# Kernel optimization log

Hardware: AMD Instinct MI355X
Metric: run time of the kernel (lower is better)

The kernel has to match this reference:

```python
import jax, jax.numpy as jnp
import numpy as np

B, T, E, H = 4, 1024, 512, 8


def setup_inputs() -> dict:
    key = jax.random.key(0)
    ks = jax.random.split(key, 8)
    s = 1.0 / np.sqrt(E)
    return {
        "x": jax.random.normal(ks[0], (B, T, E), dtype=jnp.float32),
        "mask": jnp.zeros((B, T, T), dtype=jnp.float32),
        "Wk": jax.random.uniform(ks[1], (H * E, E), minval=-s, maxval=s, dtype=jnp.float32),
        "Wq": jax.random.uniform(ks[2], (H * E, E), minval=-s, maxval=s, dtype=jnp.float32),
        "Wv": jax.random.uniform(ks[3], (H * E, E), minval=-s, maxval=s, dtype=jnp.float32),
        "Wu": jax.random.uniform(ks[4], (E, H * E), minval=-s, maxval=s, dtype=jnp.float32),
        "bu": jnp.zeros((E,), dtype=jnp.float32),
        "heads": H,
    }


def reference(x, mask, Wk, Wq, Wv, Wu, bu, heads):
    b, t, e = x.shape
    h = heads
    # Projections: torch Linear computes x @ W.T; output features laid out as [h, e]
    k = (x @ Wk.T).reshape(b, t, h, e).transpose(0, 2, 1, 3)  # [b,h,t,e]
    q = (x @ Wq.T).reshape(b, t, h, e).transpose(0, 2, 1, 3)
    v = (x @ Wv.T).reshape(b, t, h, e).transpose(0, 2, 1, 3)
    dot = jnp.einsum("bhqe,bhke->bhqk", q, k) / jnp.sqrt(jnp.float32(e))
    # mask repeat_interleave over b*h == broadcast over heads; subtracted additively
    att = jax.nn.softmax(dot - mask[:, None, :, :], axis=-1)
    out = jnp.einsum("bhqk,bhke->bhqe", att, v)  # [b,h,t,e]
    out = out.transpose(0, 2, 1, 3).reshape(b, t, h * e)
    return out @ Wu.T + bu
```

## Files before the change

kernel.cpp:

```cpp
#include <hip/hip_runtime.h>
#include <hip/hip_bf16.h>


typedef short bf16x8 __attribute__((ext_vector_type(8)));
typedef float f32x4 __attribute__((ext_vector_type(4)));
typedef unsigned short u16x8 __attribute__((ext_vector_type(8)));

__device__ __forceinline__ unsigned short f2bf(float f) {
  unsigned int u = __float_as_uint(f);
  u += 0x7FFFu + ((u >> 16) & 1u);
  return (unsigned short)(u >> 16);
}
__device__ __forceinline__ float bf2f(unsigned short s) {
  return __uint_as_float(((unsigned int)s) << 16);
}

typedef const __attribute__((address_space(1))) unsigned int* gas1_t;
typedef __attribute__((address_space(3))) unsigned int* las3_t;

__device__ __forceinline__ void gload16(const unsigned short* g, unsigned short* l) {
  __builtin_amdgcn_global_load_lds((gas1_t)g, (las3_t)l, 16, 0, 0);
}

__device__ __forceinline__ void store_val(unsigned short* p, float v) { *p = f2bf(v); }
__device__ __forceinline__ void store_val(float* p, float v) { *p = v; }

template<typename OutT>
__global__ __launch_bounds__(512, 1) void gemm_bt2(
    const unsigned short* __restrict__ A, const unsigned short* __restrict__ B,
    OutT* __restrict__ C,
    int K, int lda, int ldb, int ldc, int zshift,
    long long sAb, long long sAh, long long sBb, long long sBh,
    long long sCb, long long sCh, float alpha)
{
  const int tid  = threadIdx.x;
  const int lane = tid & 63;
  const int wave = tid >> 6;
  const int l15 = lane & 15, lhi = lane >> 4;
  const int wm = wave >> 2, wn = wave & 3;

  const int nx = gridDim.x, nxy = gridDim.x * gridDim.y;
  const int nwg = nxy * gridDim.z;
  int flat = blockIdx.x + nx * blockIdx.y + nxy * blockIdx.z;
  flat = (flat & 7) * (nwg >> 3) + (flat >> 3);
  const int bz = flat / nxy;
  const int rem = flat - bz * nxy;
  const int by = rem / nx;
  const int bx = rem - by * nx;

  const int bb = bz >> zshift, hh = bz & ((1 << zshift) - 1);
  const long long m0 = (long long)by * 256;
  const long long n0 = (long long)bx * 256;

  const unsigned short* Ab = A + bb * sAb + hh * sAh;
  const unsigned short* Bb = B + bb * sBb + hh * sBh;

  __shared__ __align__(16) unsigned short lds[49152];

  const unsigned short* gA[2];
  const unsigned short* gB[2];
  int fidx[2];
#pragma unroll
  for (int c = 0; c < 2; ++c) {
    const int f = c * 8 + wave;
    fidx[c] = f;
    gA[c] = Ab + (size_t)(m0 + f * 16 + l15) * lda + lhi * 8;
    gB[c] = Bb + (size_t)(n0 + f * 16 + l15) * ldb + lhi * 8;
  }

  auto stage = [&](int n, int p) {
    unsigned short* dst = lds + p * 16384;
    const int ko = n * 32;
#pragma unroll
    for (int c = 0; c < 2; ++c) {
      gload16(gA[c] + ko, dst + fidx[c] * 512);
      gload16(gB[c] + ko, dst + 8192 + fidx[c] * 512);
    }
  };

  f32x4 acc[8][4];
#pragma unroll
  for (int m = 0; m < 8; ++m)
#pragma unroll
    for (int n = 0; n < 4; ++n) acc[m][n] = (f32x4){0.f, 0.f, 0.f, 0.f};

  const int nt = K >> 5;
  stage(0, 0);
  stage(1, 1);
  asm volatile("s_waitcnt vmcnt(4)" ::: "memory");
  __builtin_amdgcn_sched_barrier(0);
  __builtin_amdgcn_s_barrier();

  for (int t = 0; t < nt; ++t) {
    const bool pref = (t + 2 < nt);
    if (pref) stage(t + 2, (t + 2) % 3);
    const unsigned short* base = lds + (t % 3) * 16384;
    bf16x8 af[8], bf[4];
#pragma unroll
    for (int mf = 0; mf < 8; ++mf)
      af[mf] = *(const bf16x8*)(base + (wm * 8 + mf) * 512 + lane * 8);
#pragma unroll
    for (int nf = 0; nf < 4; ++nf)
      bf[nf] = *(const bf16x8*)(base + 8192 + (wn * 4 + nf) * 512 + lane * 8);
    __builtin_amdgcn_s_setprio(1);
#pragma unroll
    for (int mf = 0; mf < 8; ++mf)
#pragma unroll
      for (int nf = 0; nf < 4; ++nf)
        acc[mf][nf] = __builtin_amdgcn_mfma_f32_16x16x32_bf16(af[mf], bf[nf], acc[mf][nf], 0, 0, 0);
    __builtin_amdgcn_s_setprio(0);
    if (pref) asm volatile("s_waitcnt vmcnt(4)" ::: "memory");
    else      asm volatile("s_waitcnt vmcnt(0)" ::: "memory");
    __builtin_amdgcn_sched_barrier(0);
    __builtin_amdgcn_s_barrier();
    __builtin_amdgcn_sched_barrier(0);
  }

  OutT* Cb = C + bb * sCb + hh * sCh;
#pragma unroll
  for (int mf = 0; mf < 8; ++mf) {
#pragma unroll
    for (int nf = 0; nf < 4; ++nf) {
      const long long col = n0 + wn * 64 + nf * 16 + l15;
#pragma unroll
      for (int r = 0; r < 4; ++r) {
        const long long row = m0 + wm * 128 + mf * 16 + lhi * 4 + r;
        store_val(Cb + (size_t)row * ldc + col, acc[mf][nf][r] * alpha);
      }
    }
  }
}

__global__ __launch_bounds__(256) void wtrans_kernel(
    const unsigned short* __restrict__ Wq, const unsigned short* __restrict__ Wk,
    unsigned short* __restrict__ Wqt, unsigned short* __restrict__ Wkt)
{
  __shared__ unsigned short t[64][72];
  const int k0 = blockIdx.x * 64;
  const int i0 = blockIdx.y * 64;
  const int hz = blockIdx.z;
  const int h = hz & 7;
  const unsigned short* src = (hz < 8) ? Wq : Wk;
  unsigned short* dst = (hz < 8) ? Wqt : Wkt;
  const int tid = threadIdx.x;
  const int r = tid >> 2, c16 = (tid & 3) * 16;
  const unsigned short* sp = src + (size_t)(h * 512 + k0 + r) * 512 + i0 + c16;
  u16x8 v0 = *(const u16x8*)sp;
  u16x8 v1 = *(const u16x8*)(sp + 8);
#pragma unroll
  for (int j = 0; j < 8; ++j) { t[r][c16 + j] = v0[j]; t[r][c16 + 8 + j] = v1[j]; }
  __syncthreads();
  unsigned short o[16];
#pragma unroll
  for (int j = 0; j < 16; ++j) o[j] = t[c16 + j][r];
  unsigned short* dp = dst + (size_t)h * 262144 + (size_t)(i0 + r) * 512 + k0 + c16;
  *(u16x8*)dp = *(u16x8*)o;
  *(u16x8*)(dp + 8) = *(u16x8*)(o + 8);
}

__global__ __launch_bounds__(256) void reduce_kernel(
    const float* __restrict__ P, const float* __restrict__ bias,
    float* __restrict__ out)
{
  const int i = blockIdx.x * 256 + threadIdx.x;
  const int col4 = i & 127;
  const float4* p4 = (const float4*)P + i;
  float4 s = p4[0];
#pragma unroll
  for (int z = 1; z < 8; ++z) {
    float4 v = p4[(size_t)z * 524288];
    s.x += v.x; s.y += v.y; s.z += v.z; s.w += v.w;
  }
  float4 b = ((const float4*)bias)[col4];
  s.x += b.x; s.y += b.y; s.z += b.z; s.w += b.w;
  ((float4*)out)[i] = s;
}

__global__ __launch_bounds__(256) void cast5_kernel(
    const float* __restrict__ s0, const float* __restrict__ s1,
    const float* __restrict__ s2, const float* __restrict__ s3,
    const float* __restrict__ s4, unsigned short* __restrict__ dst)
{
  const int seg = blockIdx.x >> 11;
  const int off = (blockIdx.x & 2047) * 256 + threadIdx.x;
  const float* s = s0;
  if (seg == 1) s = s1; else if (seg == 2) s = s2;
  else if (seg == 3) s = s3; else if (seg == 4) s = s4;
  float4 v = ((const float4*)s)[off];
  ushort4 o;
  o.x = f2bf(v.x); o.y = f2bf(v.y); o.z = f2bf(v.z); o.w = f2bf(v.w);
  ((ushort4*)dst)[(size_t)seg * 524288 + off] = o;
}

__global__ __launch_bounds__(256) void softmax_kernel(
    unsigned short* __restrict__ S, const float* __restrict__ mask)
{
  const int wave = threadIdx.x >> 6;
  const int lane = threadIdx.x & 63;
  const long long row = (long long)blockIdx.x * 4 + wave;
  const int q = (int)(row & 1023);
  const int b = (int)(row >> 13);
  unsigned short* Srow = S + row * 1024;
  const float* mrow = mask + ((size_t)b * 1024 + q) * 1024;

  u16x8 sv0 = ((const u16x8*)Srow)[lane * 2];
  u16x8 sv1 = ((const u16x8*)Srow)[lane * 2 + 1];
  float mk[16];
  const float4* m4 = (const float4*)mrow + lane * 4;
#pragma unroll
  for (int t = 0; t < 4; ++t) {
    float4 v = m4[t];
    mk[t * 4 + 0] = v.x; mk[t * 4 + 1] = v.y; mk[t * 4 + 2] = v.z; mk[t * 4 + 3] = v.w;
  }

  float lg[16];
#pragma unroll
  for (int j = 0; j < 8; ++j) lg[j] = bf2f(sv0[j]) - mk[j];
#pragma unroll
  for (int j = 0; j < 8; ++j) lg[8 + j] = bf2f(sv1[j]) - mk[8 + j];

  float mx = lg[0];
#pragma unroll
  for (int j = 1; j < 16; ++j) mx = fmaxf(mx, lg[j]);
#pragma unroll
  for (int off = 32; off > 0; off >>= 1) mx = fmaxf(mx, __shfl_xor(mx, off));

  float ex[16], sm = 0.f;
#pragma unroll
  for (int j = 0; j < 16; ++j) { ex[j] = __expf(lg[j] - mx); sm += ex[j]; }
#pragma unroll
  for (int off = 32; off > 0; off >>= 1) sm += __shfl_xor(sm, off);
  const float rinv = 1.0f / sm;

  u16x8 o0, o1;
#pragma unroll
  for (int j = 0; j < 8; ++j) o0[j] = f2bf(ex[j] * rinv);
#pragma unroll
  for (int j = 0; j < 8; ++j) o1[j] = f2bf(ex[8 + j] * rinv);
  ((u16x8*)Srow)[lane * 2] = o0;
  ((u16x8*)Srow)[lane * 2 + 1] = o1;
}

extern "C" void kernel_launch(void* const* d_in, const int* in_sizes, int n_in,
                              void* d_out, int out_size, void* d_ws, size_t ws_size,
                              hipStream_t stream) {
  const float* x    = (const float*)d_in[0];
  const float* mask = (const float*)d_in[1];
  const float* Wk   = (const float*)d_in[2];
  const float* Wq   = (const float*)d_in[3];
  const float* Wv   = (const float*)d_in[4];
  const float* Wu   = (const float*)d_in[5];
  const float* bu   = (const float*)d_in[6];

  const size_t MB = 1024 * 1024;
  if (ws_size < 192 * MB) return;
  char* ws = (char*)d_ws;
  unsigned short* xb  = (unsigned short*)(ws + 0 * MB);
  unsigned short* Wqb = (unsigned short*)(ws + 4 * MB);
  unsigned short* Wkb = (unsigned short*)(ws + 8 * MB);
  unsigned short* Wvb = (unsigned short*)(ws + 12 * MB);
  unsigned short* Wub = (unsigned short*)(ws + 16 * MB);
  unsigned short* Wqt = (unsigned short*)(ws + 20 * MB);
  unsigned short* Wkt = (unsigned short*)(ws + 24 * MB);
  unsigned short* Nh  = (unsigned short*)(ws + 28 * MB);
  unsigned short* xM  = (unsigned short*)(ws + 32 * MB);
  unsigned short* Vt  = (unsigned short*)(ws + 64 * MB);
  unsigned short* Sb  = (unsigned short*)(ws + 96 * MB);
  unsigned short* Ob  = (unsigned short*)(ws + 160 * MB);
  float* Pk = (float*)(ws + 96 * MB);

  cast5_kernel<<<5 * 2048, 256, 0, stream>>>(x, Wq, Wk, Wv, Wu, xb);

  wtrans_kernel<<<dim3(8, 8, 16), 256, 0, stream>>>(Wqb, Wkb, Wqt, Wkt);

  gemm_bt2<unsigned short><<<dim3(2, 2, 8), 512, 0, stream>>>(
      Wkt, Wqt, Nh,
      512, 512, 512, 512, 0,
      262144LL, 0, 262144LL, 0, 262144LL, 0, 1.0f);

  gemm_bt2<unsigned short><<<dim3(2, 16, 8), 512, 0, stream>>>(
      xb, Nh, xM,
      512, 512, 512, 4096, 0,
      0, 0, 262144LL, 0, 512LL, 0, 1.0f);

  gemm_bt2<unsigned short><<<dim3(16, 16, 1), 512, 0, stream>>>(
      Wvb, xb, Vt,
      512, 512, 512, 4096, 0,
      0, 0, 0, 0, 0, 0, 1.0f);

  gemm_bt2<unsigned short><<<dim3(4, 4, 32), 512, 0, stream>>>(
      xM, xb, Sb,
      512, 4096, 512, 1024, 3,
      4194304LL, 512LL, 524288LL, 0, 8388608LL, 1048576LL,
      0.044194173824159216f);

  softmax_kernel<<<8192, 256, 0, stream>>>(Sb, mask);

  gemm_bt2<unsigned short><<<dim3(2, 4, 32), 512, 0, stream>>>(
      Sb, Vt, Ob,
      1024, 1024, 4096, 4096, 3,
      8388608LL, 1048576LL, 1024LL, 2097152LL, 4194304LL, 512LL, 1.0f);

  gemm_bt2<float><<<dim3(2, 16, 8), 512, 0, stream>>>(
      Ob, Wub, Pk,
      512, 4096, 4096, 512, 0,
      512LL, 0, 512LL, 0, 2097152LL, 0, 1.0f);

  reduce_kernel<<<2048, 256, 0, stream>>>(Pk, bu, (float*)d_out);
}
```

Before: 242.4 us.

## Fold output projection into V weights to drop the PV-then-Wu GEMM

Precomputes per-head G_h = Wu_h·Wv_h (sharing a launch with the Wq/Wk product via a second operand set selected by head index), then builds xG^T = G·x^T. Attention probabilities are multiplied directly by xG^T to produce per-head fp32 partials that the existing reduce sums, which removes the separate output-projection GEMM and the Ob intermediate. The change relies on associativity and adds a third weight transpose plus an extra 512x512x512 GEMM per head, and it changes where bf16 rounding happens.

```diff
diff --git a/kernel.cpp b/kernel.cpp
--- a/kernel.cpp
+++ b/kernel.cpp
@@ -31,7 +31,10 @@
     OutT* __restrict__ C,
     int K, int lda, int ldb, int ldc, int zshift,
     long long sAb, long long sAh, long long sBb, long long sBh,
-    long long sCb, long long sCh, float alpha)
+    long long sCb, long long sCh, float alpha,
+    const unsigned short* __restrict__ A2, const unsigned short* __restrict__ B2,
+    OutT* __restrict__ C2, int lda2,
+    long long sA2h, long long sB2h, long long sC2h, int selGE)
 {
   const int tid  = threadIdx.x;
   const int lane = tid & 63;
@@ -52,8 +55,21 @@
   const long long m0 = (long long)by * 256;
   const long long n0 = (long long)bx * 256;
 
-  const unsigned short* Ab = A + bb * sAb + hh * sAh;
-  const unsigned short* Bb = B + bb * sBb + hh * sBh;
+  const unsigned short* Ab;
+  const unsigned short* Bb;
+  OutT* Cb;
+  int ldaU = lda;
+  if (selGE >= 0 && hh >= selGE) {
+    const int h2 = hh - selGE;
+    Ab = A2 + (size_t)h2 * sA2h;
+    Bb = B2 + (size_t)h2 * sB2h;
+    Cb = C2 + (size_t)h2 * sC2h;
+    ldaU = lda2;
+  } else {
+    Ab = A + bb * sAb + hh * sAh;
+    Bb = B + bb * sBb + hh * sBh;
+    Cb = C + bb * sCb + hh * sCh;
+  }
 
   __shared__ __align__(16) unsigned short lds[49152];
 
@@ -64,7 +80,7 @@
   for (int c = 0; c < 2; ++c) {
     const int f = c * 8 + wave;
     fidx[c] = f;
-    gA[c] = Ab + (size_t)(m0 + f * 16 + l15) * lda + lhi * 8;
+    gA[c] = Ab + (size_t)(m0 + f * 16 + l15) * ldaU + lhi * 8;
     gB[c] = Bb + (size_t)(n0 + f * 16 + l15) * ldb + lhi * 8;
   }
 
@@ -116,7 +132,6 @@
     __builtin_amdgcn_sched_barrier(0);
   }
 
-  OutT* Cb = C + bb * sCb + hh * sCh;
 #pragma unroll
   for (int mf = 0; mf < 8; ++mf) {
 #pragma unroll
@@ -133,15 +148,18 @@
 
 __global__ __launch_bounds__(256) void wtrans_kernel(
     const unsigned short* __restrict__ Wq, const unsigned short* __restrict__ Wk,
-    unsigned short* __restrict__ Wqt, unsigned short* __restrict__ Wkt)
+    const unsigned short* __restrict__ Wv,
+    unsigned short* __restrict__ Wqt, unsigned short* __restrict__ Wkt,
+    unsigned short* __restrict__ Wvt)
 {
   __shared__ unsigned short t[64][72];
   const int k0 = blockIdx.x * 64;
   const int i0 = blockIdx.y * 64;
   const int hz = blockIdx.z;
   const int h = hz & 7;
-  const unsigned short* src = (hz < 8) ? Wq : Wk;
-  unsigned short* dst = (hz < 8) ? Wqt : Wkt;
+  const int w = hz >> 3;
+  const unsigned short* src = (w == 0) ? Wq : ((w == 1) ? Wk : Wv);
+  unsigned short* dst = (w == 0) ? Wqt : ((w == 1) ? Wkt : Wvt);
   const int tid = threadIdx.x;
   const int r = tid >> 2, c16 = (tid & 3) * 16;
   const unsigned short* sp = src + (size_t)(h * 512 + k0 + r) * 512 + i0 + c16;
@@ -262,49 +280,50 @@
   unsigned short* Wub = (unsigned short*)(ws + 16 * MB);
   unsigned short* Wqt = (unsigned short*)(ws + 20 * MB);
   unsigned short* Wkt = (unsigned short*)(ws + 24 * MB);
-  unsigned short* Nh  = (unsigned short*)(ws + 28 * MB);
-  unsigned short* xM  = (unsigned short*)(ws + 32 * MB);
-  unsigned short* Vt  = (unsigned short*)(ws + 64 * MB);
-  unsigned short* Sb  = (unsigned short*)(ws + 96 * MB);
-  unsigned short* Ob  = (unsigned short*)(ws + 160 * MB);
-  float* Pk = (float*)(ws + 96 * MB);
+  unsigned short* Wvt = (unsigned short*)(ws + 28 * MB);
+  unsigned short* Nh  = (unsigned short*)(ws + 32 * MB);
+  unsigned short* Gh  = (unsigned short*)(ws + 36 * MB);
+  unsigned short* xM  = (unsigned short*)(ws + 40 * MB);
+  unsigned short* xGt = (unsigned short*)(ws + 72 * MB);
+  unsigned short* Sb  = (unsigned short*)(ws + 104 * MB);
+  float* Pk = (float*)(ws + 4 * MB);
 
   cast5_kernel<<<5 * 2048, 256, 0, stream>>>(x, Wq, Wk, Wv, Wu, xb);
 
-  wtrans_kernel<<<dim3(8, 8, 16), 256, 0, stream>>>(Wqb, Wkb, Wqt, Wkt);
-
-  gemm_bt2<unsigned short><<<dim3(2, 2, 8), 512, 0, stream>>>(
+  wtrans_kernel<<<dim3(8, 8, 24), 256, 0, stream>>>(Wqb, Wkb, Wvb, Wqt, Wkt, Wvt);
+
+  gemm_bt2<unsigned short><<<dim3(2, 2, 16), 512, 0, stream>>>(
       Wkt, Wqt, Nh,
-      512, 512, 512, 512, 0,
-      262144LL, 0, 262144LL, 0, 262144LL, 0, 1.0f);
+      512, 512, 512, 512, 4,
+      0, 262144LL, 0, 262144LL, 0, 262144LL, 1.0f,
+      Wub, Wvt, Gh, 4096, 512LL, 262144LL, 262144LL, 8);
 
   gemm_bt2<unsigned short><<<dim3(2, 16, 8), 512, 0, stream>>>(
       xb, Nh, xM,
       512, 512, 512, 4096, 0,
-      0, 0, 262144LL, 0, 512LL, 0, 1.0f);
+      0, 0, 262144LL, 0, 512LL, 0, 1.0f,
+      nullptr, nullptr, nullptr, 0, 0, 0, 0, -1);
 
   gemm_bt2<unsigned short><<<dim3(16, 16, 1), 512, 0, stream>>>(
-      Wvb, xb, Vt,
+      Gh, xb, xGt,
       512, 512, 512, 4096, 0,
-      0, 0, 0, 0, 0, 0, 1.0f);
+      0, 0, 0, 0, 0, 0, 1.0f,
+      nullptr, nullptr, nullptr, 0, 0, 0, 0, -1);
 
   gemm_bt2<unsigned short><<<dim3(4, 4, 32), 512, 0, stream>>>(
       xM, xb, Sb,
       512, 4096, 512, 1024, 3,
       4194304LL, 512LL, 524288LL, 0, 8388608LL, 1048576LL,
-      0.044194173824159216f);
+      0.044194173824159216f,
+      nullptr, nullptr, nullptr, 0, 0, 0, 0, -1);
 
   softmax_kernel<<<8192, 256, 0, stream>>>(Sb, mask);
 
-  gemm_bt2<unsigned short><<<dim3(2, 4, 32), 512, 0, stream>>>(
-      Sb, Vt, Ob,
-      1024, 1024, 4096, 4096, 3,
-      8388608LL, 1048576LL, 1024LL, 2097152LL, 4194304LL, 512LL, 1.0f);
-
-  gemm_bt2<float><<<dim3(2, 16, 8), 512, 0, stream>>>(
-      Ob, Wub, Pk,
-      512, 4096, 4096, 512, 0,
-      512LL, 0, 512LL, 0, 2097152LL, 0, 1.0f);
+  gemm_bt2<float><<<dim3(2, 4, 32), 512, 0, stream>>>(
+      Sb, xGt, Pk,
+      1024, 1024, 4096, 512, 3,
+      8388608LL, 1048576LL, 1024LL, 2097152LL, 524288LL, 2097152LL, 1.0f,
+      nullptr, nullptr, nullptr, 0, 0, 0, 0, -1);
 
   reduce_kernel<<<2048, 256, 0, stream>>>(Pk, bu, (float*)d_out);
 }
```

Result: faster. 224.7 us (-7.3%).
